# Kernel tuning notes

Hardware: AMD Instinct MI355X
Metric: run time of the kernel (lower is better)

Reference implementation:

```python
import jax, jax.numpy as jnp
import numpy as np

_SCAN_CHUNK = 32


def _causal_decay_scan(x, decay, init):
    """Inclusive scan out[t] = decay*out[t-1] + x[t], chunked closed form.
    x: [B,H,T,D], decay: [1,H,1], init: [B,H,D]. Returns [B,H,T,D]."""
    B, H, T, D = x.shape
    C = min(_SCAN_CHUNK, T)
    assert T % C == 0
    nC = T // C
    log_decay = jnp.log(jnp.clip(decay.astype(jnp.float32), 1e-8, None))  # [1,H,1]
    c_idx = jnp.arange(C, dtype=jnp.float32)
    log_p = log_decay[..., None] * c_idx.reshape(1, 1, C, 1)              # [1,H,C,1]
    p = jnp.exp(log_p)
    inv_p = jnp.exp(-log_p)
    init_p = jnp.exp(log_decay[..., None] * (c_idx + 1.0).reshape(1, 1, C, 1))
    # [nC, B, H, C, D] so lax.scan chains chunk states causally
    xc = x.reshape(B, H, nC, C, D).transpose(2, 0, 1, 3, 4).astype(jnp.float32)

    def step(state, chunk):  # state [B,H,D], chunk [B,H,C,D]
        cs = jnp.cumsum(chunk * inv_p, axis=2)
        out = cs * p + state[:, :, None, :] * init_p
        return out[:, :, -1, :], out

    _, outs = jax.lax.scan(step, init.astype(jnp.float32), xc)
    return outs.transpose(1, 2, 0, 3, 4).reshape(B, H, T, D).astype(x.dtype)


def _phi(x):
    return jax.nn.elu(x) + 1.0


def setup_inputs() -> dict:
    key = jax.random.key(0)
    ks = jax.random.split(key, 5)
    B, T, hidden, H = 4, 4096, 1024, 16
    s = 1.0 / np.sqrt(hidden)
    x = jax.random.normal(ks[0], (B, T, hidden), dtype=jnp.float32)
    Wqkv = jax.random.normal(ks[1], (3 * hidden, hidden), dtype=jnp.float32) * s
    Wout = jax.random.normal(ks[2], (hidden, hidden), dtype=jnp.float32) * s
    Wgate = jax.random.normal(ks[3], (hidden, hidden), dtype=jnp.float32) * s
    bgate = jnp.zeros((hidden,), dtype=jnp.float32)
    logit = float(np.log(0.95 / 0.05))  # sigmoid(logit) == 0.95
    decay_param = jnp.full((H,), logit, dtype=jnp.float32)
    return {"x": x, "Wqkv": Wqkv, "Wout": Wout, "Wgate": Wgate,
            "bgate": bgate, "decay_param": decay_param}


def reference(x, Wqkv, Wout, Wgate, bgate, decay_param):
    B, T, hidden = x.shape
    H = decay_param.shape[0]
    D = hidden // H
    qkv = x @ Wqkv.T                       # [B,T,3*hidden]
    q, k, v = jnp.split(qkv, 3, axis=-1)
    # [B,T,hidden] -> [B,H,T,D]
    q = q.reshape(B, T, H, D).transpose(0, 2, 1, 3)
    k = k.reshape(B, T, H, D).transpose(0, 2, 1, 3)
    v = v.reshape(B, T, H, D).transpose(0, 2, 1, 3)
    q = _phi(q)
    k = _phi(k)
    decay = jax.nn.sigmoid(decay_param).reshape(1, H, 1)
    kv_init = jnp.zeros((B, H, D), dtype=x.dtype)
    ksum_init = jnp.zeros((B, H, D), dtype=x.dtype)
    running_kv = _causal_decay_scan(k * v, decay, kv_init)
    running_ksum = _causal_decay_scan(k, decay, ksum_init)
    den = jnp.clip(jnp.sum(q * running_ksum, axis=-1, keepdims=True), 1e-6, None)
    out = q * running_kv / den             # [B,H,T,D]
    v_direct = v.transpose(0, 2, 1, 3).reshape(B, T, hidden)
    out = out.transpose(0, 2, 1, 3).reshape(B, T, hidden)
    g = jax.nn.sigmoid(out @ Wgate.T + bgate)
    out = g * out + (1.0 - g) * v_direct
    return out @ Wout.T
```

## Files before the change

### kernel.cpp

```cpp
#include <hip/hip_runtime.h>

typedef unsigned short u16;
typedef __bf16 bf16x8 __attribute__((ext_vector_type(8)));
typedef float f32x4 __attribute__((ext_vector_type(4)));

#define BB 4
#define TT 4096
#define HID 1024
#define NH 16
#define HD 64
#define BT (BB*TT)
#define NCH 128
#define LOG_NCH 7
#define CLEN (TT/NCH)

__device__ __forceinline__ float bf2f(u16 u) {
    return __uint_as_float(((unsigned)u) << 16);
}
__device__ __forceinline__ u16 f2bf(float f) {
    unsigned u = __float_as_uint(f);
    unsigned r = 0x7FFFu + ((u >> 16) & 1u);
    return (u16)((u + r) >> 16);
}
__device__ __forceinline__ float phi(float x) {
    return x > 0.f ? x + 1.f : __expf(x);
}
__device__ __forceinline__ float sigmoidf(float x) {
    return 1.f / (1.f + __expf(-x));
}
__device__ __forceinline__ float4 u4_to_f4(ushort4 u) {
    return make_float4(bf2f(u.x), bf2f(u.y), bf2f(u.z), bf2f(u.w));
}

#define CN1 (BT*HID/4)
#define CN2 (3*HID*HID/4)
#define CN3 (HID*HID/4)
#define CN4 (HID*HID/4)
__global__ void convert_all(const float4* __restrict__ x,    const float4* __restrict__ wqkv,
                            const float4* __restrict__ wgate, const float4* __restrict__ wout,
                            ushort4* __restrict__ xb,    ushort4* __restrict__ wqkvb,
                            ushort4* __restrict__ wgateb, ushort4* __restrict__ woutb) {
    int i = blockIdx.x * 256 + threadIdx.x;
    const float4* src; ushort4* dst; int j;
    if (i < CN1)                 { src = x;     dst = xb;     j = i; }
    else if (i < CN1+CN2)        { src = wqkv;  dst = wqkvb;  j = i - CN1; }
    else if (i < CN1+CN2+CN3)    { src = wgate; dst = wgateb; j = i - CN1 - CN2; }
    else                         { src = wout;  dst = woutb;  j = i - CN1 - CN2 - CN3; }
    float4 f = src[j];
    ushort4 u;
    u.x = f2bf(f.x); u.y = f2bf(f.y); u.z = f2bf(f.z); u.w = f2bf(f.w);
    dst[j] = u;
}

template<int EPI>
__global__ __launch_bounds__(256)
void gemm_bt(const u16* __restrict__ A, const u16* __restrict__ Bm,
             int M, int N, int K, void* __restrict__ Cout,
             const float* __restrict__ bg,
             const u16* __restrict__ attn,
             const u16* __restrict__ qkv)
{
    __shared__ u16 As[128 * 64];
    __shared__ u16 Bs[128 * 64];
    const int tid  = threadIdx.x;
    const int wave = tid >> 6;
    const int lane = tid & 63;
    const int m0 = blockIdx.y * 128;
    const int n0 = blockIdx.x * 128;
    const int mw = (wave & 1) * 64;
    const int nw = (wave >> 1) * 64;
    const int r16 = lane & 15;

    f32x4 acc[4][4];
    #pragma unroll
    for (int i = 0; i < 4; ++i)
        #pragma unroll
        for (int j = 0; j < 4; ++j)
            acc[i][j] = (f32x4){0.f, 0.f, 0.f, 0.f};

    for (int k0 = 0; k0 < K; k0 += 64) {
        #pragma unroll
        for (int i = 0; i < 4; ++i) {
            int s   = i * 4 + wave;
            int idx = s * 64 + lane;
            int pr  = idx >> 3;
            int pc  = idx & 7;
            int lc  = pc ^ (pr & 7);
            const u16* gA = A  + (size_t)(m0 + pr) * K + k0 + lc * 8;
            const u16* gB = Bm + (size_t)(n0 + pr) * K + k0 + lc * 8;
            __builtin_amdgcn_global_load_lds(
                (const __attribute__((address_space(1))) void*)gA,
                (__attribute__((address_space(3))) void*)&As[s * 512], 16, 0, 0);
            __builtin_amdgcn_global_load_lds(
                (const __attribute__((address_space(1))) void*)gB,
                (__attribute__((address_space(3))) void*)&Bs[s * 512], 16, 0, 0);
        }
        __syncthreads();
        #pragma unroll
        for (int s2 = 0; s2 < 2; ++s2) {
            const int lcq = s2 * 4 + (lane >> 4);
            const int pcq = lcq ^ (r16 & 7);
            bf16x8 af[4], bq[4];
            #pragma unroll
            for (int i = 0; i < 4; ++i)
                af[i] = *(const bf16x8*)&As[(mw + i * 16 + r16) * 64 + pcq * 8];
            #pragma unroll
            for (int j = 0; j < 4; ++j)
                bq[j] = *(const bf16x8*)&Bs[(nw + j * 16 + r16) * 64 + pcq * 8];
            #pragma unroll
            for (int i = 0; i < 4; ++i)
                #pragma unroll
                for (int j = 0; j < 4; ++j)
                    acc[i][j] = __builtin_amdgcn_mfma_f32_16x16x32_bf16(af[i], bq[j], acc[i][j], 0, 0, 0);
        }
        __syncthreads();
    }

    #pragma unroll
    for (int i = 0; i < 4; ++i) {
        int rowb = m0 + mw + i * 16 + (lane >> 4) * 4;
        #pragma unroll
        for (int j = 0; j < 4; ++j) {
            int col = n0 + nw + j * 16 + r16;
            #pragma unroll
            for (int r = 0; r < 4; ++r) {
                float v = acc[i][j][r];
                size_t row = (size_t)(rowb + r);
                if (EPI == 0) {
                    ((u16*)Cout)[row * N + col] = f2bf(v);
                } else if (EPI == 1) {
                    float g  = sigmoidf(v + bg[col]);
                    float at = bf2f(attn[row * HID + col]);
                    float vd = bf2f(qkv[row * (3 * HID) + 2 * HID + col]);
                    ((u16*)Cout)[row * HID + col] = f2bf(g * at + (1.f - g) * vd);
                } else {
                    ((float*)Cout)[row * N + col] = v;
                }
            }
        }
    }
}

template<int EPI>
__global__ __launch_bounds__(256)
void gemm_bt_sm(const u16* __restrict__ A, const u16* __restrict__ Bm,
                int M, int N, int K, void* __restrict__ Cout,
                const float* __restrict__ bg,
                const u16* __restrict__ attn,
                const u16* __restrict__ qkv)
{
    __shared__ u16 As[64 * 64];
    __shared__ u16 Bs[128 * 64];
    const int tid  = threadIdx.x;
    const int wave = tid >> 6;
    const int lane = tid & 63;
    const int m0 = blockIdx.y * 64;
    const int n0 = blockIdx.x * 128;
    const int mw = (wave & 1) * 32;
    const int nw = (wave >> 1) * 64;
    const int r16 = lane & 15;

    f32x4 acc[2][4];
    #pragma unroll
    for (int i = 0; i < 2; ++i)
        #pragma unroll
        for (int j = 0; j < 4; ++j)
            acc[i][j] = (f32x4){0.f, 0.f, 0.f, 0.f};

    for (int k0 = 0; k0 < K; k0 += 64) {
        #pragma unroll
        for (int i = 0; i < 4; ++i) {
            int s   = i * 4 + wave;
            int idx = s * 64 + lane;
            int pr  = idx >> 3;
            int pc  = idx & 7;
            int lc  = pc ^ (pr & 7);
            const u16* gB = Bm + (size_t)(n0 + pr) * K + k0 + lc * 8;
            __builtin_amdgcn_global_load_lds(
                (const __attribute__((address_space(1))) void*)gB,
                (__attribute__((address_space(3))) void*)&Bs[s * 512], 16, 0, 0);
            if (i < 2) {
                const u16* gA = A + (size_t)(m0 + pr) * K + k0 + lc * 8;
                __builtin_amdgcn_global_load_lds(
                    (const __attribute__((address_space(1))) void*)gA,
                    (__attribute__((address_space(3))) void*)&As[s * 512], 16, 0, 0);
            }
        }
        __syncthreads();
        #pragma unroll
        for (int s2 = 0; s2 < 2; ++s2) {
            const int lcq = s2 * 4 + (lane >> 4);
            const int pcq = lcq ^ (r16 & 7);
            bf16x8 af[2], bq[4];
            #pragma unroll
            for (int i = 0; i < 2; ++i)
                af[i] = *(const bf16x8*)&As[(mw + i * 16 + r16) * 64 + pcq * 8];
            #pragma unroll
            for (int j = 0; j < 4; ++j)
                bq[j] = *(const bf16x8*)&Bs[(nw + j * 16 + r16) * 64 + pcq * 8];
            #pragma unroll
            for (int i = 0; i < 2; ++i)
                #pragma unroll
                for (int j = 0; j < 4; ++j)
                    acc[i][j] = __builtin_amdgcn_mfma_f32_16x16x32_bf16(af[i], bq[j], acc[i][j], 0, 0, 0);
        }
        __syncthreads();
    }

    #pragma unroll
    for (int i = 0; i < 2; ++i) {
        int rowb = m0 + mw + i * 16 + (lane >> 4) * 4;
        #pragma unroll
        for (int j = 0; j < 4; ++j) {
            int col = n0 + nw + j * 16 + r16;
            #pragma unroll
            for (int r = 0; r < 4; ++r) {
                float v = acc[i][j][r];
                size_t row = (size_t)(rowb + r);
                if (EPI == 1) {
                    float g  = sigmoidf(v + bg[col]);
                    float at = bf2f(attn[row * HID + col]);
                    float vd = bf2f(qkv[row * (3 * HID) + 2 * HID + col]);
                    ((u16*)Cout)[row * HID + col] = f2bf(g * at + (1.f - g) * vd);
                } else {
                    ((float*)Cout)[row * N + col] = v;
                }
            }
        }
    }
}

__global__ void scan_finals(const u16* __restrict__ qkv, const float* __restrict__ decay_param,
                            float* __restrict__ ckv, float* __restrict__ cks) {
    int g  = blockIdx.x * 16 + (threadIdx.x >> 4);
    int sl = threadIdx.x & 15;
    int c = g & (NCH - 1);
    int h = (g >> LOG_NCH) & (NH - 1);
    int b = g >> (LOG_NCH + 4);
    float decay = sigmoidf(decay_param[h]);
    const u16* kp = qkv + (size_t)(b * TT + c * CLEN) * (3 * HID) + HID + h * HD + sl * 4;
    float4 skv = make_float4(0.f, 0.f, 0.f, 0.f);
    float4 sks = make_float4(0.f, 0.f, 0.f, 0.f);
    for (int t = 0; t < CLEN; ++t) {
        float4 k = u4_to_f4(*(const ushort4*)kp);
        float4 v = u4_to_f4(*(const ushort4*)(kp + HID));
        k.x = phi(k.x); k.y = phi(k.y); k.z = phi(k.z); k.w = phi(k.w);
        skv.x = decay * skv.x + k.x * v.x;  skv.y = decay * skv.y + k.y * v.y;
        skv.z = decay * skv.z + k.z * v.z;  skv.w = decay * skv.w + k.w * v.w;
        sks.x = decay * sks.x + k.x;        sks.y = decay * sks.y + k.y;
        sks.z = decay * sks.z + k.z;        sks.w = decay * sks.w + k.w;
        kp += 3 * HID;
    }
    *(float4*)(ckv + (size_t)g * 64 + sl * 4) = skv;
    *(float4*)(cks + (size_t)g * 64 + sl * 4) = sks;
}

__global__ void scan_prefix(float* __restrict__ ckv, float* __restrict__ cks,
                            const float* __restrict__ decay_param) {
    int bh = blockIdx.x;
    int h  = bh & (NH - 1);
    int lane = threadIdx.x;
    float decay = sigmoidf(decay_param[h]);
    float dC = powf(decay, (float)CLEN);
    float* pkv = ckv + (size_t)bh * NCH * 64 + lane;
    float* pks = cks + (size_t)bh * NCH * 64 + lane;
    float fkv = 0.f, fks = 0.f;
    for (int c = 0; c < NCH; ++c) {
        float lkv = pkv[c * 64], lks = pks[c * 64];
        pkv[c * 64] = fkv; pks[c * 64] = fks;
        fkv = fkv * dC + lkv;
        fks = fks * dC + lks;
    }
}

__global__ void scan_apply(const u16* __restrict__ qkv, const float* __restrict__ decay_param,
                           const float* __restrict__ ckv, const float* __restrict__ cks,
                           u16* __restrict__ attn) {
    int g  = blockIdx.x * 16 + (threadIdx.x >> 4);
    int sl = threadIdx.x & 15;
    int c = g & (NCH - 1);
    int h = (g >> LOG_NCH) & (NH - 1);
    int b = g >> (LOG_NCH + 4);
    float decay = sigmoidf(decay_param[h]);
    float4 skv = *(const float4*)(ckv + (size_t)g * 64 + sl * 4);
    float4 sks = *(const float4*)(cks + (size_t)g * 64 + sl * 4);
    const u16* qp = qkv + (size_t)(b * TT + c * CLEN) * (3 * HID) + h * HD + sl * 4;
    u16* op = attn + (size_t)(b * TT + c * CLEN) * HID + h * HD + sl * 4;
    for (int t = 0; t < CLEN; ++t) {
        float4 q = u4_to_f4(*(const ushort4*)qp);
        float4 k = u4_to_f4(*(const ushort4*)(qp + HID));
        float4 v = u4_to_f4(*(const ushort4*)(qp + 2 * HID));
        q.x = phi(q.x); q.y = phi(q.y); q.z = phi(q.z); q.w = phi(q.w);
        k.x = phi(k.x); k.y = phi(k.y); k.z = phi(k.z); k.w = phi(k.w);
        skv.x = decay * skv.x + k.x * v.x;  skv.y = decay * skv.y + k.y * v.y;
        skv.z = decay * skv.z + k.z * v.z;  skv.w = decay * skv.w + k.w * v.w;
        sks.x = decay * sks.x + k.x;        sks.y = decay * sks.y + k.y;
        sks.z = decay * sks.z + k.z;        sks.w = decay * sks.w + k.w;
        float s = q.x * sks.x + q.y * sks.y + q.z * sks.z + q.w * sks.w;
        s += __shfl_xor(s, 8);
        s += __shfl_xor(s, 4);
        s += __shfl_xor(s, 2);
        s += __shfl_xor(s, 1);
        float inv = 1.f / fmaxf(s, 1e-6f);
        ushort4 o;
        o.x = f2bf(q.x * skv.x * inv); o.y = f2bf(q.y * skv.y * inv);
        o.z = f2bf(q.z * skv.z * inv); o.w = f2bf(q.w * skv.w * inv);
        *(ushort4*)op = o;
        qp += 3 * HID;
        op += HID;
    }
}

extern "C" void kernel_launch(void* const* d_in, const int* in_sizes, int n_in,
                              void* d_out, int out_size, void* d_ws, size_t ws_size,
                              hipStream_t stream) {
    const float* x     = (const float*)d_in[0];
    const float* Wqkv  = (const float*)d_in[1];
    const float* Wout  = (const float*)d_in[2];
    const float* Wgate = (const float*)d_in[3];
    const float* bgate = (const float*)d_in[4];
    const float* decay = (const float*)d_in[5];

    u16* xb     = (u16*)d_ws;
    u16* wqkvb  = xb    + (size_t)BT * HID;
    u16* wgateb = wqkvb + (size_t)3 * HID * HID;
    u16* woutb  = wgateb + (size_t)HID * HID;
    u16* qkvb   = woutb + (size_t)HID * HID;
    u16* out2b  = qkvb  + (size_t)BT * 3 * HID;
    float* ckv  = (float*)(out2b + (size_t)BT * HID);
    float* cks  = ckv + (size_t)BB * NH * NCH * HD;
    u16* attnb  = xb;

    convert_all<<<(CN1 + CN2 + CN3 + CN4) / 256, 256, 0, stream>>>(
        (const float4*)x, (const float4*)Wqkv, (const float4*)Wgate, (const float4*)Wout,
        (ushort4*)xb, (ushort4*)wqkvb, (ushort4*)wgateb, (ushort4*)woutb);

    gemm_bt<0><<<dim3(3 * HID / 128, BT / 128), 256, 0, stream>>>(
        xb, wqkvb, BT, 3 * HID, HID, qkvb, nullptr, nullptr, nullptr);

    scan_finals<<<BB * NH * NCH / 16, 256, 0, stream>>>(qkvb, decay, ckv, cks);
    scan_prefix<<<BB * NH, 64, 0, stream>>>(ckv, cks, decay);
    scan_apply<<<BB * NH * NCH / 16, 256, 0, stream>>>(qkvb, decay, ckv, cks, attnb);

    gemm_bt_sm<1><<<dim3(HID / 128, BT / 64), 256, 0, stream>>>(
        attnb, wgateb, BT, HID, HID, out2b, bgate, attnb, qkvb);

    gemm_bt_sm<2><<<dim3(HID / 128, BT / 64), 256, 0, stream>>>(
        out2b, woutb, BT, HID, HID, d_out, nullptr, nullptr, nullptr);
}
```

Measured before the change: 400.1 us.

## Replace GEMMs with 256x256 double-buffered LDS-prefetch kernel

All three projection GEMMs now use one kernel with 256x256 tiles and 512 threads. It double-buffers the A/B LDS tiles, prefetching the K-tile two steps ahead with explicit vmcnt waits and barriers, and raises wave priority around the MFMA bursts. The goal is to hide global-load latency behind matrix math and to raise arithmetic intensity per block. In exchange it uses 128KB of LDS, which caps occupancy at one block per CU. The two hidden-size GEMMs also drop to only 256 blocks, so load balance depends on the CU count.

```diff
diff --git a/kernel.cpp b/kernel.cpp
--- a/kernel.cpp
+++ b/kernel.cpp
@@ -53,177 +53,133 @@
 }
 
 template<int EPI>
-__global__ __launch_bounds__(256)
-void gemm_bt(const u16* __restrict__ A, const u16* __restrict__ Bm,
+__global__ __launch_bounds__(512, 2)
+void gemm256(const u16* __restrict__ A, const u16* __restrict__ Bm,
              int M, int N, int K, void* __restrict__ Cout,
              const float* __restrict__ bg,
              const u16* __restrict__ attn,
              const u16* __restrict__ qkv)
 {
-    __shared__ u16 As[128 * 64];
-    __shared__ u16 Bs[128 * 64];
+    __shared__ u16 As[2][256 * 64];
+    __shared__ u16 Bs[2][256 * 64];
     const int tid  = threadIdx.x;
     const int wave = tid >> 6;
     const int lane = tid & 63;
-    const int m0 = blockIdx.y * 128;
-    const int n0 = blockIdx.x * 128;
-    const int mw = (wave & 1) * 64;
-    const int nw = (wave >> 1) * 64;
-    const int r16 = lane & 15;
-
-    f32x4 acc[4][4];
+    const int r16  = lane & 15;
+    const int m0 = blockIdx.y * 256;
+    const int n0 = blockIdx.x * 256;
+    const int wm = (wave & 1) * 128;
+    const int wn = (wave >> 1) * 64;
+
+    f32x4 acc[8][4];
     #pragma unroll
-    for (int i = 0; i < 4; ++i)
+    for (int i = 0; i < 8; ++i)
         #pragma unroll
         for (int j = 0; j < 4; ++j)
             acc[i][j] = (f32x4){0.f, 0.f, 0.f, 0.f};
 
-    for (int k0 = 0; k0 < K; k0 += 64) {
-        #pragma unroll
-        for (int i = 0; i < 4; ++i) {
-            int s   = i * 4 + wave;
+    auto STAGE = [&](int k0, int buf) {
+        #pragma unroll
+        for (int j = 0; j < 4; ++j) {
+            int s   = j * 8 + wave;
             int idx = s * 64 + lane;
             int pr  = idx >> 3;
-            int pc  = idx & 7;
-            int lc  = pc ^ (pr & 7);
+            int lc  = (idx & 7) ^ (pr & 7);
             const u16* gA = A  + (size_t)(m0 + pr) * K + k0 + lc * 8;
             const u16* gB = Bm + (size_t)(n0 + pr) * K + k0 + lc * 8;
             __builtin_amdgcn_global_load_lds(
                 (const __attribute__((address_space(1))) void*)gA,
-                (__attribute__((address_space(3))) void*)&As[s * 512], 16, 0, 0);
+                (__attribute__((address_space(3))) void*)&As[buf][s * 512], 16, 0, 0);
             __builtin_amdgcn_global_load_lds(
                 (const __attribute__((address_space(1))) void*)gB,
-                (__attribute__((address_space(3))) void*)&Bs[s * 512], 16, 0, 0);
-        }
-        __syncthreads();
-        #pragma unroll
-        for (int s2 = 0; s2 < 2; ++s2) {
-            const int lcq = s2 * 4 + (lane >> 4);
-            const int pcq = lcq ^ (r16 & 7);
-            bf16x8 af[4], bq[4];
+                (__attribute__((address_space(3))) void*)&Bs[buf][s * 512], 16, 0, 0);
+        }
+    };
+
+    auto COMPUTE = [&](int buf) {
+        bf16x8 bq[4][2];
+        #pragma unroll
+        for (int j = 0; j < 4; ++j) {
             #pragma unroll
-            for (int i = 0; i < 4; ++i)
-                af[i] = *(const bf16x8*)&As[(mw + i * 16 + r16) * 64 + pcq * 8];
+            for (int ks = 0; ks < 2; ++ks) {
+                int lcq = ks * 4 + (lane >> 4);
+                int pcq = lcq ^ (r16 & 7);
+                bq[j][ks] = *(const bf16x8*)&Bs[buf][(wn + j * 16 + r16) * 64 + pcq * 8];
+            }
+        }
+        #pragma unroll
+        for (int rh = 0; rh < 2; ++rh) {
+            bf16x8 af[4][2];
             #pragma unroll
-            for (int j = 0; j < 4; ++j)
-                bq[j] = *(const bf16x8*)&Bs[(nw + j * 16 + r16) * 64 + pcq * 8];
+            for (int i = 0; i < 4; ++i) {
+                #pragma unroll
+                for (int ks = 0; ks < 2; ++ks) {
+                    int lcq = ks * 4 + (lane >> 4);
+                    int pcq = lcq ^ (r16 & 7);
+                    af[i][ks] = *(const bf16x8*)&As[buf][(wm + rh * 64 + i * 16 + r16) * 64 + pcq * 8];
+                }
+            }
+            __builtin_amdgcn_s_setprio(1);
             #pragma unroll
             for (int i = 0; i < 4; ++i)
                 #pragma unroll
                 for (int j = 0; j < 4; ++j)
-                    acc[i][j] = __builtin_amdgcn_mfma_f32_16x16x32_bf16(af[i], bq[j], acc[i][j], 0, 0, 0);
-        }
-        __syncthreads();
+                    #pragma unroll
+                    for (int ks = 0; ks < 2; ++ks)
+                        acc[rh * 4 + i][j] = __builtin_amdgcn_mfma_f32_16x16x32_bf16(
+                            af[i][ks], bq[j][ks], acc[rh * 4 + i][j], 0, 0, 0);
+            __builtin_amdgcn_s_setprio(0);
+        }
+    };
+
+    const int nt = K >> 6;
+    STAGE(0, 0);
+    STAGE(64, 1);
+    asm volatile("s_waitcnt vmcnt(8)" ::: "memory");
+    __builtin_amdgcn_sched_barrier(0);
+    __builtin_amdgcn_s_barrier();
+    __builtin_amdgcn_sched_barrier(0);
+
+    for (int t = 0; t < nt; ++t) {
+        COMPUTE(t & 1);
+        if (t + 1 < nt) {
+            __builtin_amdgcn_sched_barrier(0);
+            __builtin_amdgcn_s_barrier();
+            __builtin_amdgcn_sched_barrier(0);
+            if (t + 2 < nt) {
+                STAGE((t + 2) << 6, t & 1);
+                asm volatile("s_waitcnt vmcnt(8)" ::: "memory");
+            } else {
+                asm volatile("s_waitcnt vmcnt(0)" ::: "memory");
+            }
+            __builtin_amdgcn_sched_barrier(0);
+            __builtin_amdgcn_s_barrier();
+            __builtin_amdgcn_sched_barrier(0);
+        }
     }
 
     #pragma unroll
-    for (int i = 0; i < 4; ++i) {
-        int rowb = m0 + mw + i * 16 + (lane >> 4) * 4;
-        #pragma unroll
-        for (int j = 0; j < 4; ++j) {
-            int col = n0 + nw + j * 16 + r16;
+    for (int rh = 0; rh < 2; ++rh) {
+        #pragma unroll
+        for (int i = 0; i < 4; ++i) {
+            int rowb = m0 + wm + rh * 64 + i * 16 + (lane >> 4) * 4;
             #pragma unroll
-            for (int r = 0; r < 4; ++r) {
-                float v = acc[i][j][r];
-                size_t row = (size_t)(rowb + r);
-                if (EPI == 0) {
-                    ((u16*)Cout)[row * N + col] = f2bf(v);
-                } else if (EPI == 1) {
-                    float g  = sigmoidf(v + bg[col]);
-                    float at = bf2f(attn[row * HID + col]);
-                    float vd = bf2f(qkv[row * (3 * HID) + 2 * HID + col]);
-                    ((u16*)Cout)[row * HID + col] = f2bf(g * at + (1.f - g) * vd);
-                } else {
-                    ((float*)Cout)[row * N + col] = v;
-                }
-            }
-        }
-    }
-}
-
-template<int EPI>
-__global__ __launch_bounds__(256)
-void gemm_bt_sm(const u16* __restrict__ A, const u16* __restrict__ Bm,
-                int M, int N, int K, void* __restrict__ Cout,
-                const float* __restrict__ bg,
-                const u16* __restrict__ attn,
-                const u16* __restrict__ qkv)
-{
-    __shared__ u16 As[64 * 64];
-    __shared__ u16 Bs[128 * 64];
-    const int tid  = threadIdx.x;
-    const int wave = tid >> 6;
-    const int lane = tid & 63;
-    const int m0 = blockIdx.y * 64;
-    const int n0 = blockIdx.x * 128;
-    const int mw = (wave & 1) * 32;
-    const int nw = (wave >> 1) * 64;
-    const int r16 = lane & 15;
-
-    f32x4 acc[2][4];
-    #pragma unroll
-    for (int i = 0; i < 2; ++i)
-        #pragma unroll
-        for (int j = 0; j < 4; ++j)
-            acc[i][j] = (f32x4){0.f, 0.f, 0.f, 0.f};
-
-    for (int k0 = 0; k0 < K; k0 += 64) {
-        #pragma unroll
-        for (int i = 0; i < 4; ++i) {
-            int s   = i * 4 + wave;
-            int idx = s * 64 + lane;
-            int pr  = idx >> 3;
-            int pc  = idx & 7;
-            int lc  = pc ^ (pr & 7);
-            const u16* gB = Bm + (size_t)(n0 + pr) * K + k0 + lc * 8;
-            __builtin_amdgcn_global_load_lds(
-                (const __attribute__((address_space(1))) void*)gB,
-                (__attribute__((address_space(3))) void*)&Bs[s * 512], 16, 0, 0);
-            if (i < 2) {
-                const u16* gA = A + (size_t)(m0 + pr) * K + k0 + lc * 8;
-                __builtin_amdgcn_global_load_lds(
-                    (const __attribute__((address_space(1))) void*)gA,
-                    (__attribute__((address_space(3))) void*)&As[s * 512], 16, 0, 0);
-            }
-        }
-        __syncthreads();
-        #pragma unroll
-        for (int s2 = 0; s2 < 2; ++s2) {
-            const int lcq = s2 * 4 + (lane >> 4);
-            const int pcq = lcq ^ (r16 & 7);
-            bf16x8 af[2], bq[4];
-            #pragma unroll
-            for (int i = 0; i < 2; ++i)
-                af[i] = *(const bf16x8*)&As[(mw + i * 16 + r16) * 64 + pcq * 8];
-            #pragma unroll
-            for (int j = 0; j < 4; ++j)
-                bq[j] = *(const bf16x8*)&Bs[(nw + j * 16 + r16) * 64 + pcq * 8];
-            #pragma unroll
-            for (int i = 0; i < 2; ++i)
+            for (int j = 0; j < 4; ++j) {
+                int col = n0 + wn + j * 16 + r16;
                 #pragma unroll
-                for (int j = 0; j < 4; ++j)
-                    acc[i][j] = __builtin_amdgcn_mfma_f32_16x16x32_bf16(af[i], bq[j], acc[i][j], 0, 0, 0);
-        }
-        __syncthreads();
-    }
-
-    #pragma unroll
-    for (int i = 0; i < 2; ++i) {
-        int rowb = m0 + mw + i * 16 + (lane >> 4) * 4;
-        #pragma unroll
-        for (int j = 0; j < 4; ++j) {
-            int col = n0 + nw + j * 16 + r16;
-            #pragma unroll
-            for (int r = 0; r < 4; ++r) {
-                float v = acc[i][j][r];
-                size_t row = (size_t)(rowb + r);
-                if (EPI == 1) {
-                    float g  = sigmoidf(v + bg[col]);
-                    float at = bf2f(attn[row * HID + col]);
-                    float vd = bf2f(qkv[row * (3 * HID) + 2 * HID + col]);
-                    ((u16*)Cout)[row * HID + col] = f2bf(g * at + (1.f - g) * vd);
-                } else {
-                    ((float*)Cout)[row * N + col] = v;
+                for (int r = 0; r < 4; ++r) {
+                    float v = acc[rh * 4 + i][j][r];
+                    size_t row = (size_t)(rowb + r);
+                    if (EPI == 0) {
+                        ((u16*)Cout)[row * N + col] = f2bf(v);
+                    } else if (EPI == 1) {
+                        float g  = sigmoidf(v + bg[col]);
+                        float at = bf2f(attn[row * HID + col]);
+                        float vd = bf2f(qkv[row * (3 * HID) + 2 * HID + col]);
+                        ((u16*)Cout)[row * HID + col] = f2bf(g * at + (1.f - g) * vd);
+                    } else {
+                        ((float*)Cout)[row * N + col] = v;
+                    }
                 }
             }
         }
@@ -335,16 +291,16 @@
         (const float4*)x, (const float4*)Wqkv, (const float4*)Wgate, (const float4*)Wout,
         (ushort4*)xb, (ushort4*)wqkvb, (ushort4*)wgateb, (ushort4*)woutb);
 
-    gemm_bt<0><<<dim3(3 * HID / 128, BT / 128), 256, 0, stream>>>(
+    gemm256<0><<<dim3(3 * HID / 256, BT / 256), 512, 0, stream>>>(
         xb, wqkvb, BT, 3 * HID, HID, qkvb, nullptr, nullptr, nullptr);
 
     scan_finals<<<BB * NH * NCH / 16, 256, 0, stream>>>(qkvb, decay, ckv, cks);
     scan_prefix<<<BB * NH, 64, 0, stream>>>(ckv, cks, decay);
     scan_apply<<<BB * NH * NCH / 16, 256, 0, stream>>>(qkvb, decay, ckv, cks, attnb);
 
-    gemm_bt_sm<1><<<dim3(HID / 128, BT / 64), 256, 0, stream>>>(
+    gemm256<1><<<dim3(HID / 256, BT / 256), 512, 0, stream>>>(
         attnb, wgateb, BT, HID, HID, out2b, bgate, attnb, qkvb);
 
-    gemm_bt_sm<2><<<dim3(HID / 128, BT / 64), 256, 0, stream>>>(
+    gemm256<2><<<dim3(HID / 256, BT / 256), 512, 0, stream>>>(
         out2b, woutb, BT, HID, HID, d_out, nullptr, nullptr, nullptr);
 }
```

Measured after the change: 376.8 us. 1.06x faster.
